# Kernel optimization log

Measured on AMD Instinct MI355X. Metric: run time of the kernel, lower is better.

## Reference

```python
import jax, jax.numpy as jnp
import numpy as np

EPS = 1e-5


def conv1x1(x, w):
    # x: (N, C, V, T), w: (O, C) -> (N, O, V, T)
    return jnp.einsum('ncvt,oc->novt', x, w)


def batchnorm2d(y, gamma, beta):
    # training-mode BN over (N, V, T) per channel, biased variance (torch semantics)
    mean = jnp.mean(y, axis=(0, 2, 3), keepdims=True)
    var = jnp.mean((y - mean) ** 2, axis=(0, 2, 3), keepdims=True)
    yhat = (y - mean) * jax.lax.rsqrt(var + EPS)
    return yhat * gamma[None, :, None, None] + beta[None, :, None, None]


def spatial_g(x, wg1, wg2):
    # learned adjacency: softmax over last dim of (N, T, V, V)
    a1 = conv1x1(x, wg1)  # (N, O, V, T)
    a2 = conv1x1(x, wg2)  # (N, O, V, T)
    g = jnp.einsum('novt,nout->ntvu', a1, a2)  # (N, T, V, V)
    return jax.nn.softmax(g, axis=-1)


def gcn_unit(x, g, w1, w2, gamma, beta):
    # message passing: g (N,T,V,V) applied over joint dim of x (N,C,V,T)
    x1 = jnp.einsum('ntvu,ncut->ncvt', g, x)
    y = conv1x1(x1, w1) + conv1x1(x, w2)
    return jax.nn.relu(batchnorm2d(y, gamma, beta))


def setup_inputs() -> dict:
    key = jax.random.key(0)
    ks = jax.random.split(key, 12)
    N, C, V, T = 64, 64, 25, 128
    dims = [64, 64, 128, 256]
    gp = 16
    s = 0.05
    inp = {
        'x': jax.random.normal(ks[0], (N, C, V, T), jnp.float32),
        'wg1': jax.random.normal(ks[1], (gp, dims[0]), jnp.float32) * s,
        'wg2': jax.random.normal(ks[2], (gp, dims[0]), jnp.float32) * s,
        'w11': jax.random.normal(ks[3], (dims[1], dims[0]), jnp.float32) * s,
        'w12': jax.random.normal(ks[4], (dims[1], dims[0]), jnp.float32) * s,
        'gamma1': jnp.ones((dims[1],), jnp.float32),
        'beta1': jnp.zeros((dims[1],), jnp.float32),
        'w21': jax.random.normal(ks[5], (dims[2], dims[1]), jnp.float32) * s,
        'w22': jax.random.normal(ks[6], (dims[2], dims[1]), jnp.float32) * s,
        'gamma2': jnp.ones((dims[2],), jnp.float32),
        'beta2': jnp.zeros((dims[2],), jnp.float32),
        'w31': jax.random.normal(ks[7], (dims[3], dims[2]), jnp.float32) * s,
        'w32': jax.random.normal(ks[8], (dims[3], dims[2]), jnp.float32) * s,
        'gamma3': jnp.ones((dims[3],), jnp.float32),
        'beta3': jnp.zeros((dims[3],), jnp.float32),
    }
    return inp


def reference(x, wg1, wg2, w11, w12, gamma1, beta1, w21, w22, gamma2, beta2,
              w31, w32, gamma3, beta3):
    g = spatial_g(x, wg1, wg2)                       # shared adjacency (N,T,V,V)
    x = gcn_unit(x, g, w11, w12, gamma1, beta1)      # (N, 64, V, T)
    x = gcn_unit(x, g, w21, w22, gamma2, beta2)      # (N, 128, V, T)
    x = gcn_unit(x, g, w31, w32, gamma3, beta3)      # (N, 256, V, T)
    return x, g
```

## Files before the change

kernel.cpp:

```cpp
#include <hip/hip_runtime.h>
#include <cstdint>

#define V_ 25
#define T_ 128
#define VT_ 3200
#define NVTF_ 204800.0f

typedef unsigned short ushort_t;
typedef __attribute__((ext_vector_type(8))) short s16x8;
typedef __attribute__((ext_vector_type(4))) float f32x4;

#define SW(r, ch) ((ch) ^ ((r) & 7) ^ (((r) >> 3) & 7))

__device__ __forceinline__ ushort_t f2bf(float f) {
    union { float f; unsigned u; } v; v.f = f;
    unsigned r = v.u + 0x7FFFu + ((v.u >> 16) & 1u);
    return (ushort_t)(r >> 16);
}
__device__ __forceinline__ float bf2f(ushort_t h) {
    union { unsigned u; float f; } v; v.u = ((unsigned)h) << 16;
    return v.f;
}
__device__ __forceinline__ unsigned cvtpk(float lo, float hi) {
    unsigned r;
    asm volatile("v_cvt_pk_bf16_f32 %0, %1, %2" : "=v"(r) : "v"(lo), "v"(hi));
    return r;
}
__device__ __forceinline__ void gload16(const void* g, void* l) {
    __builtin_amdgcn_global_load_lds((const __attribute__((address_space(1))) void*)g,
                                     (__attribute__((address_space(3))) void*)l, 16, 0, 0);
}

__global__ __launch_bounds__(128) void k_a(const float* __restrict__ x,
        const float* __restrict__ wg1, const float* __restrict__ wg2,
        ushort_t* __restrict__ a1, ushort_t* __restrict__ a2,
        ushort_t* __restrict__ xb,
        const float* __restrict__ w11, const float* __restrict__ w12,
        const float* __restrict__ w21, const float* __restrict__ w22,
        const float* __restrict__ w31, const float* __restrict__ w32,
        ushort_t* __restrict__ Wc) {
    int b = blockIdx.x; int n = b / V_; int v = b % V_;
    int t = threadIdx.x;
    int wi = b * 128 + t;
    if (wi < 90112) {
        float wv;
        if (wi < 8192) {
            int o = wi >> 7, k = wi & 127;
            wv = (k < 64) ? w11[o * 64 + k] : w12[o * 64 + k - 64];
        } else if (wi < 24576) {
            int j = wi - 8192; int o = j >> 7, k = j & 127;
            wv = (k < 64) ? w21[o * 64 + k] : w22[o * 64 + k - 64];
        } else {
            int j = wi - 24576; int o = j >> 8, k = j & 255;
            wv = (k < 128) ? w31[o * 128 + k] : w32[o * 128 + k - 128];
        }
        Wc[wi] = f2bf(wv);
    }
    __shared__ float w1s[1024], w2s[1024];
    for (int i = threadIdx.x; i < 1024; i += 128) { w1s[i] = wg1[i]; w2s[i] = wg2[i]; }
    __syncthreads();
    float s1[16], s2[16];
    #pragma unroll
    for (int o = 0; o < 16; o++) { s1[o] = 0.f; s2[o] = 0.f; }
    s16x8 xs[8];
    const float* xp = x + (size_t)n * 204800 + v * T_ + t;
    #pragma unroll
    for (int c = 0; c < 64; c++) {
        float xv = xp[(size_t)c * VT_];
        xs[c >> 3][c & 7] = (short)f2bf(xv);
        #pragma unroll
        for (int o = 0; o < 16; o++) {
            s1[o] = fmaf(w1s[o*64+c], xv, s1[o]);
            s2[o] = fmaf(w2s[o*64+c], xv, s2[o]);
        }
    }
    size_t abase = (size_t)n * 51200 + v * T_ + t;
    #pragma unroll
    for (int o = 0; o < 16; o++) {
        a1[abase + (size_t)o * VT_] = f2bf(s1[o]);
        a2[abase + (size_t)o * VT_] = f2bf(s2[o]);
    }
    ushort_t* cp = xb + (size_t)(n * VT_ + v * T_ + t) * 64;
    #pragma unroll
    for (int ch = 0; ch < 8; ch++) *(s16x8*)(cp + ch * 8) = xs[ch];
}

__global__ __launch_bounds__(256) void k_g(const ushort_t* __restrict__ a1,
        const ushort_t* __restrict__ a2, float* __restrict__ g,
        ushort_t* __restrict__ gb) {
    int n = blockIdx.x >> 3; int t0 = (blockIdx.x & 7) * 16;
    __shared__ float A1s[6400], A2s[6400];
    for (int i = threadIdx.x; i < 6400; i += 256) {
        int o = i / 400; int r = i % 400; int v = r >> 4; int tt = r & 15;
        size_t ga = (size_t)n * 51200 + (size_t)o * VT_ + v * T_ + t0 + tt;
        A1s[i] = bf2f(a1[ga]);
        A2s[i] = bf2f(a2[ga]);
    }
    __syncthreads();
    for (int r = threadIdx.x; r < 400; r += 256) {
        int v = r >> 4; int tt = r & 15;
        float a1r[16];
        #pragma unroll
        for (int o = 0; o < 16; o++) a1r[o] = A1s[o*400 + v*16 + tt];
        float gr[25];
        float mx = -1e30f;
        for (int u = 0; u < 25; u++) {
            float s = 0.f;
            #pragma unroll
            for (int o = 0; o < 16; o++) s = fmaf(a1r[o], A2s[o*400 + u*16 + tt], s);
            gr[u] = s; mx = fmaxf(mx, s);
        }
        float sum = 0.f;
        for (int u = 0; u < 25; u++) { gr[u] = __expf(gr[u] - mx); sum += gr[u]; }
        float inv = 1.f / sum;
        float* gp = g + ((size_t)(n * T_ + t0 + tt) * V_ + v) * V_;
        ushort_t* gbp = gb + ((size_t)((n * 128 + t0 + tt) * 25 + v)) * 32;
        for (int u = 0; u < 25; u++) {
            float val = gr[u] * inv;
            gp[u] = val;
            gbp[u] = f2bf(val);
        }
        #pragma unroll
        for (int u = 25; u < 32; u++) gbp[u] = 0;
    }
}

template<int C, bool BNB, bool XBSRC, int TOUT, int OPASS>
__global__ __launch_bounds__(256) void k_fgemm(
        const ushort_t* __restrict__ Wc, const ushort_t* __restrict__ ysrc,
        const ushort_t* __restrict__ gb,
        const float* __restrict__ bns, const float* __restrict__ bnb,
        ushort_t* __restrict__ yt,
        float* __restrict__ psum, float* __restrict__ psq) {
    constexpr int K2 = 2 * C;
    constexpr int KSTEPS = K2 / 32;
    constexpr int NC8 = C / 8;
    constexpr int NCT = C / 16;
    constexpr int HKS = C / 32;
    constexpr int MROWS = 100;
    constexpr int MI = 7;
    constexpr int XBYTES = (TOUT == 0) ? 14400 : 16;
    __shared__ __align__(16) ushort_t YS[MROWS * C];
    __shared__ __align__(16) ushort_t MPo[MROWS * C];
    __shared__ __align__(16) char XTRA[XBYTES];
    ushort_t* Lw = (ushort_t*)XTRA;

    int n = blockIdx.y, mb = blockIdx.x;
    int m0 = mb * MROWS, tb = mb * 4;
    int tid = threadIdx.x, w = tid >> 6, lane = tid & 63;
    int l15 = lane & 15, g4 = lane >> 4;

    const ushort_t* gbase = gb + ((size_t)((n * 128 + tb + w) * 25)) * 32;
    s16x8 aG0 = *(const s16x8*)(gbase + (size_t)(l15) * 32 + g4 * 8);
    s16x8 aG1 = *(const s16x8*)(gbase + (size_t)(16 + l15) * 32 + g4 * 8);

    for (int i = tid; i < MROWS * NC8; i += 256) {
        int yr = i / NC8, cc = i % NC8;
        size_t saddr;
        if (XBSRC) {
            int t = tb + yr / 25, v = yr % 25;
            saddr = (size_t)n * 204800 + (size_t)(v * 128 + t) * 64 + cc * 8;
        } else {
            saddr = ((size_t)n * VT_ + m0 + yr) * C + cc * 8;
        }
        s16x8 vv = *(const s16x8*)(ysrc + saddr);
        if (BNB) {
            int ob = cc * 8;
            float4 s0 = *(const float4*)(bns + ob), s1 = *(const float4*)(bns + ob + 4);
            float4 h0 = *(const float4*)(bnb + ob), h1 = *(const float4*)(bnb + ob + 4);
            float sc[8] = {s0.x, s0.y, s0.z, s0.w, s1.x, s1.y, s1.z, s1.w};
            float sh[8] = {h0.x, h0.y, h0.z, h0.w, h1.x, h1.y, h1.z, h1.w};
            float ff[8];
            #pragma unroll
            for (int j = 0; j < 8; j++)
                ff[j] = fmaxf(fmaf(bf2f((ushort_t)vv[j]), sc[j], sh[j]), 0.f);
            union { unsigned u[4]; s16x8 s; } U;
            U.u[0] = cvtpk(ff[0], ff[1]); U.u[1] = cvtpk(ff[2], ff[3]);
            U.u[2] = cvtpk(ff[4], ff[5]); U.u[3] = cvtpk(ff[6], ff[7]);
            vv = U.s;
        }
        *(s16x8*)(YS + ((size_t)yr * NC8 + SW(yr, cc)) * 8) = vv;
    }
    __syncthreads();
    {
        int tl = w;
        #pragma unroll
        for (int ct = 0; ct < NCT; ct++) {
            int c = ct * 16 + l15;
            int cc = c >> 3, sub = c & 7;
            s16x8 bF;
            #pragma unroll
            for (int j = 0; j < 8; j++) {
                int u = g4 * 8 + j;
                int uu = (u > 24) ? 24 : u;
                int r = tl * 25 + uu;
                bF[j] = (short)YS[((size_t)r * NC8 + SW(r, cc)) * 8 + sub];
            }
            f32x4 z = {};
            f32x4 d0 = __builtin_amdgcn_mfma_f32_16x16x32_bf16(aG0, bF, z, 0, 0, 0);
            f32x4 d1 = __builtin_amdgcn_mfma_f32_16x16x32_bf16(aG1, bF, z, 0, 0, 0);
            #pragma unroll
            for (int b = 0; b < 4; b++) {
                int v0 = g4 * 4 + b;
                int r0 = tl * 25 + v0;
                MPo[((size_t)r0 * NC8 + SW(r0, cc)) * 8 + sub] = f2bf(d0[b]);
                int v1 = 16 + g4 * 4 + b;
                if (v1 < 25) {
                    int r1 = tl * 25 + v1;
                    MPo[((size_t)r1 * NC8 + SW(r1, cc)) * 8 + sub] = f2bf(d1[b]);
                }
            }
        }
    }
    __syncthreads();
    for (int pass = 0; pass < OPASS; pass++) {
        int o0 = pass * 64;
        s16x8 aReg[KSTEPS];
        const ushort_t* ap = Wc + (size_t)(o0 + w * 16 + l15) * K2 + g4 * 8;
        #pragma unroll
        for (int ks = 0; ks < KSTEPS; ks++)
            aReg[ks] = *(const s16x8*)(ap + ks * 32);
        f32x4 acc[MI] = {};
        __builtin_amdgcn_s_setprio(1);
        #pragma unroll
        for (int ks = 0; ks < KSTEPS; ks++) {
            const ushort_t* bbase = (ks < HKS) ? MPo : YS;
            int ksl = (ks < HKS) ? ks : ks - HKS;
            #pragma unroll
            for (int mi = 0; mi < MI; mi++) {
                int r = mi * 16 + l15;
                int rr = (r < MROWS) ? r : (MROWS - 1);
                int ch = ksl * 4 + g4;
                s16x8 bF = *(const s16x8*)(bbase + ((size_t)rr * NC8 + SW(rr, ch)) * 8);
                acc[mi] = __builtin_amdgcn_mfma_f32_16x16x32_bf16(aReg[ks], bF, acc[mi], 0, 0, 0);
            }
        }
        __builtin_amdgcn_s_setprio(0);
        int p = n * 32 + mb;
        #pragma unroll
        for (int b = 0; b < 4; b++) {
            float ss = 0.f, qq = 0.f;
            #pragma unroll
            for (int mi = 0; mi < MI; mi++) {
                float v0 = acc[mi][b];
                if (mi == 6 && l15 >= 4) v0 = 0.f;
                ss += v0; qq = fmaf(v0, v0, qq);
            }
            #pragma unroll
            for (int msk = 1; msk < 16; msk <<= 1) {
                ss += __shfl_xor(ss, msk, 16);
                qq += __shfl_xor(qq, msk, 16);
            }
            if (l15 == 0) {
                int o = o0 + w * 16 + g4 * 4 + b;
                psum[(size_t)o * 2048 + p] = ss;
                psq [(size_t)o * 2048 + p] = qq;
            }
        }
        if (TOUT == 0) {
            __syncthreads();
            #pragma unroll
            for (int mi = 0; mi < MI; mi++) {
                int r = mi * 16 + l15;
                if (r < MROWS) {
                    unsigned lo = cvtpk(acc[mi][0], acc[mi][1]);
                    unsigned hi = cvtpk(acc[mi][2], acc[mi][3]);
                    *(unsigned*)(Lw + r * 72 + w * 16 + g4 * 4)     = lo;
                    *(unsigned*)(Lw + r * 72 + w * 16 + g4 * 4 + 2) = hi;
                }
            }
            __syncthreads();
            for (int i = tid; i < MROWS * 8; i += 256) {
                int r = i >> 3, oc = i & 7;
                s16x8 pk = *(const s16x8*)(Lw + r * 72 + oc * 8);
                *(s16x8*)(yt + ((size_t)n * VT_ + m0 + r) * (OPASS * 64) + o0 + oc * 8) = pk;
            }
        } else {
            int obase = n * 256 + o0 + w * 16 + g4 * 4;
            #pragma unroll
            for (int mi = 0; mi < MI; mi++) {
                int r = mi * 16 + l15;
                if (r < MROWS) {
                    #pragma unroll
                    for (int b = 0; b < 4; b++)
                        yt[(size_t)(obase + b) * VT_ + m0 + r] = f2bf(acc[mi][b]);
                }
            }
        }
    }
}

__global__ __launch_bounds__(256) void k_stats(const float* __restrict__ psum,
        const float* __restrict__ psq, const float* __restrict__ gamma,
        const float* __restrict__ beta, float* __restrict__ bns,
        float* __restrict__ bnb) {
    int o = blockIdx.x;
    float s = 0.f, q = 0.f;
    for (int i = threadIdx.x; i < 2048; i += 256) {
        s += psum[(size_t)o*2048+i]; q += psq[(size_t)o*2048+i];
    }
    __shared__ float rs[256], rq[256];
    rs[threadIdx.x] = s; rq[threadIdx.x] = q;
    __syncthreads();
    for (int st = 128; st > 0; st >>= 1) {
        if (threadIdx.x < st) { rs[threadIdx.x] += rs[threadIdx.x+st]; rq[threadIdx.x] += rq[threadIdx.x+st]; }
        __syncthreads();
    }
    if (threadIdx.x == 0) {
        float mean = rs[0] / NVTF_;
        float var = rq[0] / NVTF_ - mean * mean;
        float scale = gamma[o] * rsqrtf(var + 1e-5f);
        bns[o] = scale;
        bnb[o] = beta[o] - mean * scale;
    }
}

__global__ __launch_bounds__(256) void k_bnf(const ushort_t* __restrict__ y3,
        const float* __restrict__ bns, const float* __restrict__ bnb,
        float* __restrict__ xout) {
    __shared__ __align__(16) ushort_t L[8 * VT_];
    int n = blockIdx.y, oc = blockIdx.x;
    size_t base = (size_t)(n * 256 + oc * 8) * VT_;
    for (int i = threadIdx.x; i < 3200; i += 256)
        gload16(y3 + base + (size_t)i * 8, (char*)L + i * 16);
    __syncthreads();
    for (int i = threadIdx.x; i < 6400; i += 256) {
        int t4 = i & 31, v = (i >> 5) % 25, o = i / 800;
        int og = oc * 8 + o;
        float sc = bns[og], sh = bnb[og];
        int lb = o * VT_ + v;
        float4 f;
        f.x = fmaxf(fmaf(bf2f(L[lb + (t4*4+0)*25]), sc, sh), 0.f);
        f.y = fmaxf(fmaf(bf2f(L[lb + (t4*4+1)*25]), sc, sh), 0.f);
        f.z = fmaxf(fmaf(bf2f(L[lb + (t4*4+2)*25]), sc, sh), 0.f);
        f.w = fmaxf(fmaf(bf2f(L[lb + (t4*4+3)*25]), sc, sh), 0.f);
        *(float4*)(xout + (size_t)(n * 256 + og) * VT_ + v * T_ + t4 * 4) = f;
    }
}

extern "C" void kernel_launch(void* const* d_in, const int* in_sizes, int n_in,
                              void* d_out, int out_size, void* d_ws, size_t ws_size,
                              hipStream_t stream) {
    const float* x   = (const float*)d_in[0];
    const float* wg1 = (const float*)d_in[1];
    const float* wg2 = (const float*)d_in[2];
    const float* w11 = (const float*)d_in[3];
    const float* w12 = (const float*)d_in[4];
    const float* ga1 = (const float*)d_in[5];
    const float* be1 = (const float*)d_in[6];
    const float* w21 = (const float*)d_in[7];
    const float* w22 = (const float*)d_in[8];
    const float* ga2 = (const float*)d_in[9];
    const float* be2 = (const float*)d_in[10];
    const float* w31 = (const float*)d_in[11];
    const float* w32 = (const float*)d_in[12];
    const float* ga3 = (const float*)d_in[13];
    const float* be3 = (const float*)d_in[14];

    float* xout = (float*)d_out;
    float* gout = xout + 52428800;

    float* ws = (float*)d_ws;
    ushort_t* xb  = (ushort_t*)(ws + 0);
    ushort_t* a1  = (ushort_t*)(ws + 6553600);
    ushort_t* a2  = (ushort_t*)(ws + 8192000);
    ushort_t* y1  = (ushort_t*)(ws + 9830400);
    ushort_t* y2  = (ushort_t*)(ws + 16384000);
    ushort_t* y3  = (ushort_t*)(ws + 29491200);
    ushort_t* gb  = (ushort_t*)(ws + 55705600);
    float* psum = ws + 58982400;
    float* psq  = ws + 59506688;
    ushort_t* Wc = (ushort_t*)(ws + 60030976);
    float* bns  = ws + 60076032;
    float* bnb  = ws + 60076288;
    ushort_t* Wc1 = Wc, *Wc2 = Wc + 8192, *Wc3 = Wc + 24576;

    k_a<<<1600, 128, 0, stream>>>(x, wg1, wg2, a1, a2, xb,
                                  w11, w12, w21, w22, w31, w32, Wc);
    k_g<<<512, 256, 0, stream>>>(a1, a2, gout, gb);

    k_fgemm<64, false, true, 0, 1><<<dim3(32, 64), 256, 0, stream>>>(
        Wc1, xb, gb, nullptr, nullptr, y1, psum, psq);
    k_stats<<<64, 256, 0, stream>>>(psum, psq, ga1, be1, bns, bnb);

    k_fgemm<64, true, false, 0, 2><<<dim3(32, 64), 256, 0, stream>>>(
        Wc2, y1, gb, bns, bnb, y2, psum, psq);
    k_stats<<<128, 256, 0, stream>>>(psum, psq, ga2, be2, bns, bnb);

    k_fgemm<128, true, false, 2, 4><<<dim3(32, 64), 256, 0, stream>>>(
        Wc3, y2, gb, bns, bnb, y3, psum, psq);
    k_stats<<<256, 256, 0, stream>>>(psum, psq, ga3, be3, bns, bnb);

    k_bnf<<<dim3(32, 64), 256, 0, stream>>>(y3, bns, bnb, xout);
}
```

Before: 294.0 us.

## Fuse adjacency projection and softmax kernels, keep a1/a2 in shared memory

Merges the kernel that computes the two 1x1 projections (a1, a2) and the bf16 copy of x with the kernel that forms the V×V adjacency and softmax. Each block now handles one batch and a 16-step time slice, writes the projections straight into shared memory in fp32, and never round-trips a1/a2 through global memory or bf16. This removes one launch and the a1/a2 global write and read. In exchange it has only 512 blocks of 256 threads where there were 1600 smaller blocks, and threads 144-255 idle in the projection loop, so parallelism for that phase drops.

Result: slower. 403.1 us (+37.1%).

```diff
diff --git a/kernel.cpp b/kernel.cpp
--- a/kernel.cpp
+++ b/kernel.cpp
@@ -31,17 +31,18 @@
                                      (__attribute__((address_space(3))) void*)l, 16, 0, 0);
 }
 
-__global__ __launch_bounds__(128) void k_a(const float* __restrict__ x,
+__global__ __launch_bounds__(256) void k_ag(const float* __restrict__ x,
         const float* __restrict__ wg1, const float* __restrict__ wg2,
-        ushort_t* __restrict__ a1, ushort_t* __restrict__ a2,
-        ushort_t* __restrict__ xb,
+        ushort_t* __restrict__ xb, float* __restrict__ g, ushort_t* __restrict__ gb,
         const float* __restrict__ w11, const float* __restrict__ w12,
         const float* __restrict__ w21, const float* __restrict__ w22,
         const float* __restrict__ w31, const float* __restrict__ w32,
         ushort_t* __restrict__ Wc) {
-    int b = blockIdx.x; int n = b / V_; int v = b % V_;
-    int t = threadIdx.x;
-    int wi = b * 128 + t;
+    __shared__ float w1s[1024], w2s[1024];
+    __shared__ float A1s[6400], A2s[6400];
+    int n = blockIdx.y, t0 = blockIdx.x * 16;
+    int tid = threadIdx.x;
+    int wi = (blockIdx.y * 8 + blockIdx.x) * 256 + tid;
     if (wi < 90112) {
         float wv;
         if (wi < 8192) {
@@ -56,48 +57,36 @@
         }
         Wc[wi] = f2bf(wv);
     }
-    __shared__ float w1s[1024], w2s[1024];
-    for (int i = threadIdx.x; i < 1024; i += 128) { w1s[i] = wg1[i]; w2s[i] = wg2[i]; }
-    __syncthreads();
-    float s1[16], s2[16];
-    #pragma unroll
-    for (int o = 0; o < 16; o++) { s1[o] = 0.f; s2[o] = 0.f; }
-    s16x8 xs[8];
-    const float* xp = x + (size_t)n * 204800 + v * T_ + t;
-    #pragma unroll
-    for (int c = 0; c < 64; c++) {
-        float xv = xp[(size_t)c * VT_];
-        xs[c >> 3][c & 7] = (short)f2bf(xv);
+    for (int i = tid; i < 1024; i += 256) { w1s[i] = wg1[i]; w2s[i] = wg2[i]; }
+    __syncthreads();
+    for (int i = tid; i < 400; i += 256) {
+        int v = i >> 4, tt = i & 15;
+        float s1[16], s2[16];
+        #pragma unroll
+        for (int o = 0; o < 16; o++) { s1[o] = 0.f; s2[o] = 0.f; }
+        s16x8 xs[8];
+        const float* xp = x + (size_t)n * 204800 + v * T_ + t0 + tt;
+        #pragma unroll
+        for (int c = 0; c < 64; c++) {
+            float xv = xp[(size_t)c * VT_];
+            xs[c >> 3][c & 7] = (short)f2bf(xv);
+            #pragma unroll
+            for (int o = 0; o < 16; o++) {
+                s1[o] = fmaf(w1s[o*64+c], xv, s1[o]);
+                s2[o] = fmaf(w2s[o*64+c], xv, s2[o]);
+            }
+        }
+        ushort_t* cp = xb + (size_t)(n * VT_ + v * T_ + t0 + tt) * 64;
+        #pragma unroll
+        for (int ch = 0; ch < 8; ch++) *(s16x8*)(cp + ch * 8) = xs[ch];
         #pragma unroll
         for (int o = 0; o < 16; o++) {
-            s1[o] = fmaf(w1s[o*64+c], xv, s1[o]);
-            s2[o] = fmaf(w2s[o*64+c], xv, s2[o]);
-        }
-    }
-    size_t abase = (size_t)n * 51200 + v * T_ + t;
-    #pragma unroll
-    for (int o = 0; o < 16; o++) {
-        a1[abase + (size_t)o * VT_] = f2bf(s1[o]);
-        a2[abase + (size_t)o * VT_] = f2bf(s2[o]);
-    }
-    ushort_t* cp = xb + (size_t)(n * VT_ + v * T_ + t) * 64;
-    #pragma unroll
-    for (int ch = 0; ch < 8; ch++) *(s16x8*)(cp + ch * 8) = xs[ch];
-}
-
-__global__ __launch_bounds__(256) void k_g(const ushort_t* __restrict__ a1,
-        const ushort_t* __restrict__ a2, float* __restrict__ g,
-        ushort_t* __restrict__ gb) {
-    int n = blockIdx.x >> 3; int t0 = (blockIdx.x & 7) * 16;
-    __shared__ float A1s[6400], A2s[6400];
-    for (int i = threadIdx.x; i < 6400; i += 256) {
-        int o = i / 400; int r = i % 400; int v = r >> 4; int tt = r & 15;
-        size_t ga = (size_t)n * 51200 + (size_t)o * VT_ + v * T_ + t0 + tt;
-        A1s[i] = bf2f(a1[ga]);
-        A2s[i] = bf2f(a2[ga]);
-    }
-    __syncthreads();
-    for (int r = threadIdx.x; r < 400; r += 256) {
+            A1s[o * 400 + v * 16 + tt] = s1[o];
+            A2s[o * 400 + v * 16 + tt] = s2[o];
+        }
+    }
+    __syncthreads();
+    for (int r = tid; r < 400; r += 256) {
         int v = r >> 4; int tt = r & 15;
         float a1r[16];
         #pragma unroll
@@ -362,8 +351,6 @@
 
     float* ws = (float*)d_ws;
     ushort_t* xb  = (ushort_t*)(ws + 0);
-    ushort_t* a1  = (ushort_t*)(ws + 6553600);
-    ushort_t* a2  = (ushort_t*)(ws + 8192000);
     ushort_t* y1  = (ushort_t*)(ws + 9830400);
     ushort_t* y2  = (ushort_t*)(ws + 16384000);
     ushort_t* y3  = (ushort_t*)(ws + 29491200);
@@ -375,9 +362,8 @@
     float* bnb  = ws + 60076288;
     ushort_t* Wc1 = Wc, *Wc2 = Wc + 8192, *Wc3 = Wc + 24576;
 
-    k_a<<<1600, 128, 0, stream>>>(x, wg1, wg2, a1, a2, xb,
-                                  w11, w12, w21, w22, w31, w32, Wc);
-    k_g<<<512, 256, 0, stream>>>(a1, a2, gout, gb);
+    k_ag<<<dim3(8, 64), 256, 0, stream>>>(x, wg1, wg2, xb, gout, gb,
+                                          w11, w12, w21, w22, w31, w32, Wc);
 
     k_fgemm<64, false, true, 0, 1><<<dim3(32, 64), 256, 0, stream>>>(
         Wc1, xb, gb, nullptr, nullptr, y1, psum, psq);
```
